# Kernel tuning notes

Hardware: AMD Instinct MI355X
Metric: run time of the kernel (lower is better)

The kernel has to match this reference:

```python
import jax, jax.numpy as jnp
import numpy as np
import math

B = 16          # graphs per batch
N = 2048        # nodes per graph
F_IN = 64       # input node features
E_PER = 32768   # edges per graph
E = B * E_PER
H = 128         # hidden width (fixed by module)
C = 10          # output classes
K = math.ceil(0.8 * N)  # TopKPooling keep count per graph = 1639


def setup_inputs() -> dict:
    key = jax.random.key(0)
    ks = jax.random.split(key, 24)
    x = jax.random.normal(ks[0], (B * N, F_IN), jnp.float32)
    # intra-graph random edges (source->target), global node ids
    gid = jnp.repeat(jnp.arange(B, dtype=jnp.int32), E_PER)
    src = gid * N + jax.random.randint(ks[1], (E,), 0, N, dtype=jnp.int32)
    dst = gid * N + jax.random.randint(ks[2], (E,), 0, N, dtype=jnp.int32)

    def lin_w(k, o, i):
        return jax.random.normal(k, (o, i), jnp.float32) / jnp.sqrt(i)

    inp = dict(x=x, src=src, dst=dst)
    # GraphConv: lin_rel (with bias) on aggregated neighbors + lin_root (no bias)
    inp.update(W1_rel=lin_w(ks[3], H, F_IN), b1=jnp.zeros((H,), jnp.float32), W1_root=lin_w(ks[4], H, F_IN))
    inp.update(W2_rel=lin_w(ks[5], H, H), b2=jnp.zeros((H,), jnp.float32), W2_root=lin_w(ks[6], H, H))
    inp.update(W3_rel=lin_w(ks[7], H, H), b3=jnp.zeros((H,), jnp.float32), W3_root=lin_w(ks[8], H, H))
    inp.update(pool_w=jax.random.normal(ks[9], (H,), jnp.float32) / jnp.sqrt(H))
    inp.update(Wl1=lin_w(ks[10], 128, 256), bl1=jnp.zeros((128,), jnp.float32))
    inp.update(Wl2=lin_w(ks[11], 64, 128), bl2=jnp.zeros((64,), jnp.float32))
    inp.update(Wl3=lin_w(ks[12], C, 64), bl3=jnp.zeros((C,), jnp.float32))
    return inp


def _graph_conv(x, src, dst, W_rel, b, W_root, n_nodes, emask=None):
    # out_i = W_rel @ (sum_{j->i} x_j) + b + W_root @ x_i
    msg = x[src]
    if emask is not None:
        msg = msg * emask[:, None]
    agg = jax.ops.segment_sum(msg, dst, num_segments=n_nodes)
    return agg @ W_rel.T + b + x @ W_root.T


def _global_pools(x, n_per_graph):
    xb = x.reshape(B, n_per_graph, -1)
    return jnp.concatenate([xb.max(axis=1), xb.mean(axis=1)], axis=1)  # [B, 2F]


def reference(x, src, dst, W1_rel, b1, W1_root, W2_rel, b2, W2_root,
              W3_rel, b3, W3_root, pool_w, Wl1, bl1, Wl2, bl2, Wl3, bl3):
    n0 = B * N
    h = jax.nn.relu(_graph_conv(x, src, dst, W1_rel, b1, W1_root, n0))
    x1 = _global_pools(h, N)

    h = jax.nn.relu(_graph_conv(h, src, dst, W2_rel, b2, W2_root, n0))

    # TopKPooling(ratio=0.8): score = tanh(x@w/||w||); keep top-k per graph;
    # kept features scaled by score; edges with a dropped endpoint removed.
    score = jnp.tanh((h @ pool_w) / jnp.linalg.norm(pool_w))  # [B*N]
    top_s, top_i = jax.lax.top_k(score.reshape(B, N), K)      # [B,K]
    perm = (top_i + jnp.arange(B)[:, None] * N).reshape(-1)   # global old ids [B*K]
    h = h[perm] * top_s.reshape(-1)[:, None]                  # [B*K, H]

    n1 = B * K
    new_id = jnp.full((n0,), -1, jnp.int32).at[perm].set(jnp.arange(n1, dtype=jnp.int32))
    ns, nd = new_id[src], new_id[dst]
    keep = ((ns >= 0) & (nd >= 0)).astype(h.dtype)
    ns = jnp.where(ns >= 0, ns, 0)
    nd = jnp.where(nd >= 0, nd, 0)

    x2 = _global_pools(h, K)
    h = jax.nn.relu(_graph_conv(h, ns, nd, W3_rel, b3, W3_root, n1, emask=keep))
    x3 = _global_pools(h, K)

    z = x1 + x2 + x3
    z = jax.nn.relu(z @ Wl1.T + bl1)
    z = jax.nn.relu(z @ Wl2.T + bl2)
    return jax.nn.log_softmax(z @ Wl3.T + bl3, axis=-1)  # [B, C]
```

## Files before the change

kernel.cpp:

```cpp
#include <hip/hip_runtime.h>
#include <hip/hip_bf16.h>
#include <math.h>

#define NB 32768
#define NN 2048
#define BG 16
#define KK 1639
#define KKP 1664
#define N1 (BG*KK)
#define N1P (BG*KKP)
#define EE 524288
#define HH 128
#define FIN 64

using half8 = __attribute__((ext_vector_type(8))) _Float16;
using f32x4 = __attribute__((ext_vector_type(4))) float;

__global__ void deg_kernel(const int* __restrict__ dst, int* deg, int n) {
  int e = blockIdx.x * blockDim.x + threadIdx.x;
  if (e < n) atomicAdd(&deg[dst[e]], 1);
}

__global__ void deg2_kernel(const int* __restrict__ src, const int* __restrict__ dst,
                            const int* __restrict__ new_id, int* deg, int n) {
  int e = blockIdx.x * blockDim.x + threadIdx.x;
  if (e < n) {
    int a = new_id[src[e]], d = new_id[dst[e]];
    if (a >= 0 && d >= 0) atomicAdd(&deg[d], 1);
  }
}

__global__ void exscan_kernel(const int* __restrict__ deg, int* rs, int* cursor, int n) {
  __shared__ int wsum[16];
  __shared__ int carry;
  int t = threadIdx.x;
  int lane = t & 63, wid = t >> 6;
  if (t == 0) carry = 0;
  __syncthreads();
  int ntiles = (n + 4095) >> 12;
  for (int tile = 0; tile < ntiles; ++tile) {
    int idx = (tile << 12) + t * 4;
    int4 v4 = *(const int4*)(deg + idx);
    int v0 = (idx + 0 < n) ? v4.x : 0;
    int v1 = (idx + 1 < n) ? v4.y : 0;
    int v2 = (idx + 2 < n) ? v4.z : 0;
    int v3 = (idx + 3 < n) ? v4.w : 0;
    int s = v0 + v1 + v2 + v3;
    int pre = s;
#pragma unroll
    for (int off = 1; off < 64; off <<= 1) {
      int u = __shfl_up(pre, off, 64);
      if (lane >= off) pre += u;
    }
    if (lane == 63) wsum[wid] = pre;
    __syncthreads();
    int wbase = 0;
#pragma unroll
    for (int ww = 0; ww < 16; ++ww)
      if (ww < wid) wbase += wsum[ww];
    int ex = carry + wbase + (pre - s);
    int4 e4 = make_int4(ex, ex + v0, ex + v0 + v1, ex + v0 + v1 + v2);
    if (idx + 3 < n) {
      *(int4*)(rs + idx) = e4;
      *(int4*)(cursor + idx) = e4;
    } else {
      if (idx + 0 < n) { rs[idx + 0] = e4.x; cursor[idx + 0] = e4.x; }
      if (idx + 1 < n) { rs[idx + 1] = e4.y; cursor[idx + 1] = e4.y; }
      if (idx + 2 < n) { rs[idx + 2] = e4.z; cursor[idx + 2] = e4.z; }
    }
    int tot = 0;
    if (t == 1023) tot = ex + s;
    __syncthreads();
    if (t == 1023) carry = tot;
    __syncthreads();
  }
  if (t == 0) rs[n] = carry;
}

__global__ void scatter_kernel(const int* __restrict__ src, const int* __restrict__ dst,
                               int* cursor, int* csr, int n) {
  int e = blockIdx.x * blockDim.x + threadIdx.x;
  if (e < n) {
    int d = dst[e];
    int p = atomicAdd(&cursor[d], 1);
    csr[p] = src[e];
  }
}

__global__ void scatter2_kernel(const int* __restrict__ src, const int* __restrict__ dst,
                                const int* __restrict__ new_id, int* cursor, int* csr, int n) {
  int e = blockIdx.x * blockDim.x + threadIdx.x;
  if (e < n) {
    int a = new_id[src[e]], d = new_id[dst[e]];
    if (a >= 0 && d >= 0) {
      int p = atomicAdd(&cursor[d], 1);
      csr[p] = a;
    }
  }
}

template <int KD1, int KD2, int POOL, int SCORE>
__global__ __launch_bounds__(512, 4) void conv_mfma(
    const float* __restrict__ feat, const float* __restrict__ xr,
    const int* __restrict__ rs, const int* __restrict__ csr,
    const _Float16* __restrict__ Wh, const _Float16* __restrict__ Wl,
    const float* __restrict__ bias, float* __restrict__ out, int M, int nwg,
    float* __restrict__ pmax, float* __restrict__ psum,
    const float* __restrict__ pw, float* __restrict__ score) {
  constexpr int KTOT = KD1 + KD2;
  constexpr int NSTEP = KTOT / 32;
  constexpr int CPT = KD1 / 32;
  __shared__ _Float16 ah_lds[64 * KTOT];
  __shared__ _Float16 al_lds[64 * KTOT];
  __shared__ float sdot[64][8];
  __shared__ float swsq[8];

  int tid = threadIdx.x;
  int lane = tid & 63, wid = tid >> 6;
  int bq = nwg >> 3, br = nwg & 7, bx = blockIdx.x & 7, bi = blockIdx.x >> 3;
  int swz = (bx < br ? bx * (bq + 1) : br * (bq + 1) + (bx - br) * bq) + bi;
  int row0 = swz * 64;
  int ch0 = wid * 16;
  int col = lane & 15;
  int kseg = (lane >> 4) * 8;

  {
    int gr = tid >> 3;
    int gj = tid & 7;
    int grow = row0 + gr;
    if (grow >= M) grow = M - 1;
    const float4* fbase = (const float4*)feat + gj * CPT;
    int e0 = rs[grow], e1 = rs[grow + 1];
    f32x4 s[CPT];
#pragma unroll
    for (int j = 0; j < CPT; ++j) s[j] = (f32x4){0.f, 0.f, 0.f, 0.f};
    int e = e0;
    for (; e + 3 < e1; e += 4) {
      int c0 = csr[e], c1 = csr[e + 1], c2 = csr[e + 2], c3 = csr[e + 3];
      const float4* p0 = fbase + (size_t)c0 * (KD1 / 4);
      const float4* p1 = fbase + (size_t)c1 * (KD1 / 4);
      const float4* p2 = fbase + (size_t)c2 * (KD1 / 4);
      const float4* p3 = fbase + (size_t)c3 * (KD1 / 4);
      float4 v0[CPT], v1[CPT], v2[CPT], v3[CPT];
#pragma unroll
      for (int j = 0; j < CPT; ++j) { v0[j] = p0[j]; v1[j] = p1[j]; v2[j] = p2[j]; v3[j] = p3[j]; }
#pragma unroll
      for (int j = 0; j < CPT; ++j) {
        s[j] += (f32x4){v0[j].x, v0[j].y, v0[j].z, v0[j].w};
        s[j] += (f32x4){v1[j].x, v1[j].y, v1[j].z, v1[j].w};
        s[j] += (f32x4){v2[j].x, v2[j].y, v2[j].z, v2[j].w};
        s[j] += (f32x4){v3[j].x, v3[j].y, v3[j].z, v3[j].w};
      }
    }
    for (; e < e1; ++e) {
      const float4* p = fbase + (size_t)csr[e] * (KD1 / 4);
#pragma unroll
      for (int j = 0; j < CPT; ++j) {
        float4 v = p[j];
        s[j] += (f32x4){v.x, v.y, v.z, v.w};
      }
    }
    int base = (gr * KTOT + gj * CPT * 4) * 2;
    int sw = (gr & 7) << 4;
#pragma unroll
    for (int h = 0; h < CPT / 2; ++h) {
      half8 vh, vl;
#pragma unroll
      for (int j = 0; j < 8; ++j) {
        float f = s[h * 2 + (j >> 2)][j & 3];
        _Float16 hi = (_Float16)f;
        vh[j] = hi;
        vl[j] = (_Float16)(f - (float)hi);
      }
      int byte = (base + h * 16) ^ sw;
      *(half8*)((char*)ah_lds + byte) = vh;
      *(half8*)((char*)al_lds + byte) = vl;
    }
  }

  for (int idx = tid; idx < 64 * KD2 / 8; idx += 512) {
    int row = idx / (KD2 / 8);
    int kc = (idx % (KD2 / 8)) * 8;
    int grow = row0 + row;
    if (grow >= M) grow = M - 1;
    const float* sp = xr + (size_t)grow * KD2 + kc;
    float4 a0 = *(const float4*)sp;
    float4 a1 = *(const float4*)(sp + 4);
    float av[8] = {a0.x, a0.y, a0.z, a0.w, a1.x, a1.y, a1.z, a1.w};
    half8 vh, vl;
#pragma unroll
    for (int j = 0; j < 8; ++j) {
      _Float16 h = (_Float16)av[j];
      vh[j] = h;
      vl[j] = (_Float16)(av[j] - (float)h);
    }
    int byte = ((row * KTOT + KD1 + kc) * 2) ^ ((row & 7) << 4);
    *(half8*)((char*)ah_lds + byte) = vh;
    *(half8*)((char*)al_lds + byte) = vl;
  }

  size_t wbase = (size_t)(ch0 + col) * KTOT + kseg;
  half8 whc = *(const half8*)(Wh + wbase);
  half8 wlc = *(const half8*)(Wl + wbase);
  __syncthreads();

  f32x4 acc[4];
#pragma unroll
  for (int rf = 0; rf < 4; ++rf) acc[rf] = (f32x4){0.f, 0.f, 0.f, 0.f};
  int r = lane & 15;
#pragma unroll
  for (int s = 0; s < NSTEP; ++s) {
    half8 whn, wln;
    if (s + 1 < NSTEP) {
      whn = *(const half8*)(Wh + wbase + (s + 1) * 32);
      wln = *(const half8*)(Wl + wbase + (s + 1) * 32);
    }
#pragma unroll
    for (int rf = 0; rf < 4; ++rf) {
      int row = rf * 16 + r;
      int byte = ((row * KTOT + s * 32 + kseg) * 2) ^ ((row & 7) << 4);
      half8 a_h = *(const half8*)((const char*)ah_lds + byte);
      half8 a_l = *(const half8*)((const char*)al_lds + byte);
      acc[rf] = __builtin_amdgcn_mfma_f32_16x16x32_f16(a_l, whc, acc[rf], 0, 0, 0);
      acc[rf] = __builtin_amdgcn_mfma_f32_16x16x32_f16(a_h, wlc, acc[rf], 0, 0, 0);
      acc[rf] = __builtin_amdgcn_mfma_f32_16x16x32_f16(a_h, whc, acc[rf], 0, 0, 0);
    }
    if (s + 1 < NSTEP) { whc = whn; wlc = wln; }
  }

  float bv = bias[ch0 + col];
  float cmax = -3.402823466e38f, csum = 0.f;
  float wcol = SCORE ? pw[ch0 + col] : 0.f;
  float pd[4][4];
  int g = 0, rowbase = 0;
  if (POOL == 2) { g = row0 / KKP; rowbase = row0 - g * KKP; }
#pragma unroll
  for (int rf = 0; rf < 4; ++rf) {
    int orow0 = row0 + rf * 16 + (lane >> 4) * 4;
#pragma unroll
    for (int rr = 0; rr < 4; ++rr) {
      int orow = orow0 + rr;
      float v = fmaxf(acc[rf][rr] + bv, 0.f);
      if (orow < M) out[(size_t)orow * HH + ch0 + col] = v;
      if (POOL == 1) { cmax = fmaxf(cmax, v); csum += v; }
      if (POOL == 2) {
        int local = rowbase + rf * 16 + (lane >> 4) * 4 + rr;
        if (local < KK) { cmax = fmaxf(cmax, v); csum += v; }
      }
      if (SCORE) pd[rf][rr] = v * wcol;
    }
  }
  if (POOL) {
    cmax = fmaxf(cmax, __shfl_xor(cmax, 16, 64)); csum += __shfl_xor(csum, 16, 64);
    cmax = fmaxf(cmax, __shfl_xor(cmax, 32, 64)); csum += __shfl_xor(csum, 32, 64);
    if ((lane >> 4) == 0) {
      if (POOL == 1) {
        int gg = row0 >> 11, sb = (row0 & 2047) >> 6;
        pmax[(gg * 32 + sb) * HH + ch0 + col] = cmax;
        psum[(gg * 32 + sb) * HH + ch0 + col] = csum;
      } else {
        int sb = rowbase >> 6;
        pmax[(g * 26 + sb) * HH + ch0 + col] = cmax;
        psum[(g * 26 + sb) * HH + ch0 + col] = csum;
      }
    }
  }
  if (SCORE) {
#pragma unroll
    for (int rf = 0; rf < 4; ++rf)
#pragma unroll
      for (int rr = 0; rr < 4; ++rr) {
        float d = pd[rf][rr];
        d += __shfl_xor(d, 1, 64); d += __shfl_xor(d, 2, 64);
        d += __shfl_xor(d, 4, 64); d += __shfl_xor(d, 8, 64);
        if (col == 0) sdot[rf * 16 + (lane >> 4) * 4 + rr][wid] = d;
      }
    float wsq = wcol * wcol;
    wsq += __shfl_xor(wsq, 1, 64); wsq += __shfl_xor(wsq, 2, 64);
    wsq += __shfl_xor(wsq, 4, 64); wsq += __shfl_xor(wsq, 8, 64);
    if (lane == 0) swsq[wid] = wsq;
    __syncthreads();
    if (tid < 64) {
      float d = 0.f, q = 0.f;
#pragma unroll
      for (int wv = 0; wv < 8; ++wv) { d += sdot[tid][wv]; q += swsq[wv]; }
      score[row0 + tid] = tanhf(d * rsqrtf(q));
    }
  }
}

__global__ void prep_weights_f16(const float* __restrict__ W1_rel, const float* __restrict__ W1_root,
                                 const float* __restrict__ W2_rel, const float* __restrict__ W2_root,
                                 const float* __restrict__ W3_rel, const float* __restrict__ W3_root,
                                 _Float16* wh1, _Float16* wl1, _Float16* wh2, _Float16* wl2,
                                 _Float16* wh3, _Float16* wl3) {
  int idx = blockIdx.x * blockDim.x + threadIdx.x;
  float v;
  _Float16* ph;
  _Float16* pl;
  int j;
  if (idx < 128 * 128) {
    j = idx;
    int o = j >> 7, k = j & 127;
    v = (k < 64) ? W1_rel[o * 64 + k] : W1_root[o * 64 + (k - 64)];
    ph = wh1; pl = wl1;
  } else if (idx < 128 * 128 + 128 * 256) {
    j = idx - 128 * 128;
    int o = j >> 8, k = j & 255;
    v = (k < 128) ? W2_rel[o * 128 + k] : W2_root[o * 128 + (k - 128)];
    ph = wh2; pl = wl2;
  } else if (idx < 128 * 128 + 2 * 128 * 256) {
    j = idx - 128 * 128 - 128 * 256;
    int o = j >> 8, k = j & 255;
    v = (k < 128) ? W3_rel[o * 128 + k] : W3_root[o * 128 + (k - 128)];
    ph = wh3; pl = wl3;
  } else {
    return;
  }
  _Float16 h = (_Float16)v;
  ph[j] = h;
  pl[j] = (_Float16)(v - (float)h);
}

__global__ void topk_kernel(const float* __restrict__ score, int* perm) {
  __shared__ unsigned long long k[NN];
  int b = blockIdx.x;
  int tid = threadIdx.x;
  for (int i = tid; i < NN; i += 1024) {
    float s = score[b * NN + i];
    unsigned u = __float_as_uint(s);
    u = (u & 0x80000000u) ? ~u : (u | 0x80000000u);
    unsigned long long key = ((unsigned long long)u << 32) | (unsigned)(NN - 1 - i);
    k[i] = ~key;
  }
  __syncthreads();
  for (int kk = 2; kk <= NN; kk <<= 1) {
    for (int j = kk >> 1; j > 0; j >>= 1) {
      for (int t = tid; t < NN; t += 1024) {
        int ixj = t ^ j;
        if (ixj > t) {
          bool up = ((t & kk) == 0);
          unsigned long long a = k[t], c = k[ixj];
          if ((a > c) == up) { k[t] = c; k[ixj] = a; }
        }
      }
      __syncthreads();
    }
  }
  for (int j = tid; j < KK; j += 1024) {
    unsigned long long key = ~k[j];
    int i = (NN - 1) - (int)(key & 0xffffffffu);
    perm[b * KK + j] = b * NN + i;
  }
}

__global__ void h3_kernel(const float4* __restrict__ h2, const int* __restrict__ perm,
                          const float* __restrict__ score, float4* __restrict__ h3,
                          int* __restrict__ new_id) {
  int idx = blockIdx.x * blockDim.x + threadIdx.x;
  if (idx < N1 * 32) {
    int g = idx >> 5, c = idx & 31;
    int b = g / KK, j = g - b * KK;
    int p = perm[g];
    if (c == 0) new_id[p] = b * KKP + j;
    float s = score[p];
    float4 v = h2[(size_t)p * 32 + c];
    v.x *= s; v.y *= s; v.z *= s; v.w *= s;
    h3[(size_t)(b * KKP + j) * 32 + c] = v;
  }
}

__global__ void pool2_kernel(const float* __restrict__ h, float* pmax, float* psum) {
  int b = blockIdx.x / 26, s = blockIdx.x % 26;
  int f = threadIdx.x;
  int r0 = s * 64, r1 = min(KK, r0 + 64);
  float m = -3.402823466e38f, sum = 0.f;
  for (int r = r0; r < r1; ++r) {
    float v = h[(size_t)(b * KKP + r) * HH + f];
    m = fmaxf(m, v);
    sum += v;
  }
  pmax[(b * 26 + s) * HH + f] = m;
  psum[(b * 26 + s) * HH + f] = sum;
}

__global__ void mlp_kernel(const float* __restrict__ pm1, const float* __restrict__ ps1,
                           const float* __restrict__ pm2, const float* __restrict__ ps2,
                           const float* __restrict__ pm3, const float* __restrict__ ps3,
                           const float* __restrict__ Wl1, const float* __restrict__ bl1,
                           const float* __restrict__ Wl2, const float* __restrict__ bl2,
                           const float* __restrict__ Wl3, const float* __restrict__ bl3,
                           float* out) {
  __shared__ float z[256], a1[128], a2[64], a3[10], red[2];
  int b = blockIdx.x, t = threadIdx.x;
  float m1 = -3.402823466e38f, m2 = m1, m3 = m1;
  float s1 = 0.f, s2 = 0.f, s3 = 0.f;
  for (int s = 0; s < 32; ++s) {
    int o = (b * 32 + s) * 128 + t;
    m1 = fmaxf(m1, pm1[o]); s1 += ps1[o];
  }
  for (int s = 0; s < 26; ++s) {
    int o = (b * 26 + s) * 128 + t;
    m2 = fmaxf(m2, pm2[o]); s2 += ps2[o];
    m3 = fmaxf(m3, pm3[o]); s3 += ps3[o];
  }
  z[t] = m1 + m2 + m3;
  z[128 + t] = s1 * (1.f / NN) + (s2 + s3) * (1.f / KK);
  __syncthreads();
  {
    float acc = bl1[t];
    for (int q = 0; q < 256; ++q) acc = fmaf(Wl1[t * 256 + q], z[q], acc);
    a1[t] = fmaxf(acc, 0.f);
  }
  __syncthreads();
  if (t < 64) {
    float acc = bl2[t];
    for (int q = 0; q < 128; ++q) acc = fmaf(Wl2[t * 128 + q], a1[q], acc);
    a2[t] = fmaxf(acc, 0.f);
  }
  __syncthreads();
  if (t < 10) {
    float acc = bl3[t];
    for (int q = 0; q < 64; ++q) acc = fmaf(Wl3[t * 64 + q], a2[q], acc);
    a3[t] = acc;
  }
  __syncthreads();
  if (t == 0) {
    float m = a3[0];
    for (int i = 1; i < 10; ++i) m = fmaxf(m, a3[i]);
    float s = 0.f;
    for (int i = 0; i < 10; ++i) s += expf(a3[i] - m);
    red[0] = m;
    red[1] = logf(s);
  }
  __syncthreads();
  if (t < 10) out[b * 10 + t] = a3[t] - red[0] - red[1];
}

extern "C" void kernel_launch(void* const* d_in, const int* in_sizes, int n_in,
                              void* d_out, int out_size, void* d_ws, size_t ws_size,
                              hipStream_t stream) {
  const float* x       = (const float*)d_in[0];
  const int*   src     = (const int*)d_in[1];
  const int*   dst     = (const int*)d_in[2];
  const float* W1_rel  = (const float*)d_in[3];
  const float* b1      = (const float*)d_in[4];
  const float* W1_root = (const float*)d_in[5];
  const float* W2_rel  = (const float*)d_in[6];
  const float* b2      = (const float*)d_in[7];
  const float* W2_root = (const float*)d_in[8];
  const float* W3_rel  = (const float*)d_in[9];
  const float* b3      = (const float*)d_in[10];
  const float* W3_root = (const float*)d_in[11];
  const float* pool_w  = (const float*)d_in[12];
  const float* Wl1     = (const float*)d_in[13];
  const float* bl1     = (const float*)d_in[14];
  const float* Wl2     = (const float*)d_in[15];
  const float* bl2     = (const float*)d_in[16];
  const float* Wl3     = (const float*)d_in[17];
  const float* bl3     = (const float*)d_in[18];
  float* out = (float*)d_out;

  char* w = (char*)d_ws;
  size_t off = 0;
  auto alloc = [&](size_t bytes) -> char* {
    off = (off + 255) & ~(size_t)255;
    char* p = w + off;
    off += bytes;
    return p;
  };
  int* degs     = (int*)alloc((NB + N1P + 4096) * 4);
  int* deg1     = degs;
  int* deg2     = degs + NB;
  int* rs1      = (int*)alloc((NB + 1) * 4);
  int* cursor1  = (int*)alloc(NB * 4);
  int* csr1     = (int*)alloc((size_t)EE * 4);
  int* rs2      = (int*)alloc((N1P + 1) * 4);
  int* cursor2  = (int*)alloc(N1P * 4);
  int* csr2     = (int*)alloc((size_t)EE * 4);
  int* new_id   = (int*)alloc(NB * 4);
  int* perm     = (int*)alloc(N1 * 4);
  _Float16* wh1 = (_Float16*)alloc(128 * 128 * 2);
  _Float16* wl1 = (_Float16*)alloc(128 * 128 * 2);
  _Float16* wh2 = (_Float16*)alloc(128 * 256 * 2);
  _Float16* wl2 = (_Float16*)alloc(128 * 256 * 2);
  _Float16* wh3 = (_Float16*)alloc(128 * 256 * 2);
  _Float16* wl3 = (_Float16*)alloc(128 * 256 * 2);
  float* bufA   = (float*)alloc((size_t)NB * HH * 4);
  float* bufB   = (float*)alloc((size_t)NB * HH * 4);
  float* score  = (float*)alloc(NB * 4);
  float* pm1    = (float*)alloc(BG * 32 * HH * 4);
  float* ps1    = (float*)alloc(BG * 32 * HH * 4);
  float* pm2    = (float*)alloc(BG * 26 * HH * 4);
  float* ps2    = (float*)alloc(BG * 26 * HH * 4);
  float* pm3    = (float*)alloc(BG * 26 * HH * 4);
  float* ps3    = (float*)alloc(BG * 26 * HH * 4);
  if (off > ws_size) return;

  const int TB = 256;
  const int egrid = (EE + TB - 1) / TB;

  hipMemsetAsync(degs, 0, (NB + N1P + 4096) * 4, stream);
  hipMemsetAsync(new_id, 0xFF, NB * 4, stream);

  prep_weights_f16<<<(128 * 128 + 2 * 128 * 256 + TB - 1) / TB, TB, 0, stream>>>(
      W1_rel, W1_root, W2_rel, W2_root, W3_rel, W3_root, wh1, wl1, wh2, wl2, wh3, wl3);

  deg_kernel<<<egrid, TB, 0, stream>>>(dst, deg1, EE);
  exscan_kernel<<<1, 1024, 0, stream>>>(deg1, rs1, cursor1, NB);
  scatter_kernel<<<egrid, TB, 0, stream>>>(src, dst, cursor1, csr1, EE);

  conv_mfma<64, 64, 1, 0><<<NB / 64, 512, 0, stream>>>(
      x, x, rs1, csr1, wh1, wl1, b1, bufA, NB, NB / 64, pm1, ps1, nullptr, nullptr);

  conv_mfma<128, 128, 0, 1><<<NB / 64, 512, 0, stream>>>(
      bufA, bufA, rs1, csr1, wh2, wl2, b2, bufB, NB, NB / 64, nullptr, nullptr, pool_w, score);

  topk_kernel<<<BG, 1024, 0, stream>>>(score, perm);
  h3_kernel<<<(N1 * 32 + TB - 1) / TB, TB, 0, stream>>>((const float4*)bufB, perm, score,
                                                        (float4*)bufA, new_id);
  pool2_kernel<<<BG * 26, 128, 0, stream>>>(bufA, pm2, ps2);

  deg2_kernel<<<egrid, TB, 0, stream>>>(src, dst, new_id, deg2, EE);
  exscan_kernel<<<1, 1024, 0, stream>>>(deg2, rs2, cursor2, N1P);
  scatter2_kernel<<<egrid, TB, 0, stream>>>(src, dst, new_id, cursor2, csr2, EE);

  conv_mfma<128, 128, 2, 0><<<N1P / 64, 512, 0, stream>>>(
      bufA, bufA, rs2, csr2, wh3, wl3, b3, bufB, N1P, N1P / 64, pm3, ps3, nullptr, nullptr);

  mlp_kernel<<<BG, 128, 0, stream>>>(pm1, ps1, pm2, ps2, pm3, ps3,
                                     Wl1, bl1, Wl2, bl2, Wl3, bl3, out);
}
```

Before: 275.0 us.

## Restructure neighbor gather so each wave cooperatively aggregates rows with coalesced loads

Replaces the per-thread gather, where 8 threads per row each summed a fixed slice of features serially over all edges, with a wave-per-8-rows scheme. In the new scheme lanes split into feature chunks and edge subgroups, and partial sums are combined with cross-lane shuffles. Each edge's feature row is now read by contiguous lanes, which coalesces loads and spreads the edge loop across lanes to cut per-row latency on long adjacency lists. The cost is more shuffles and wave-serialized row processing, and some lanes sit idle when a row has few edges.

Result: no change. 277.1 us (+0.7%).

```diff
diff --git a/kernel.cpp b/kernel.cpp
--- a/kernel.cpp
+++ b/kernel.cpp
@@ -14,6 +14,7 @@
 #define FIN 64
 
 using half8 = __attribute__((ext_vector_type(8))) _Float16;
+using half4 = __attribute__((ext_vector_type(4))) _Float16;
 using f32x4 = __attribute__((ext_vector_type(4))) float;
 
 __global__ void deg_kernel(const int* __restrict__ dst, int* deg, int n) {
@@ -109,7 +110,6 @@
     const float* __restrict__ pw, float* __restrict__ score) {
   constexpr int KTOT = KD1 + KD2;
   constexpr int NSTEP = KTOT / 32;
-  constexpr int CPT = KD1 / 32;
   __shared__ _Float16 ah_lds[64 * KTOT];
   __shared__ _Float16 al_lds[64 * KTOT];
   __shared__ float sdot[64][8];
@@ -125,56 +125,53 @@
   int kseg = (lane >> 4) * 8;
 
   {
-    int gr = tid >> 3;
-    int gj = tid & 7;
-    int grow = row0 + gr;
-    if (grow >= M) grow = M - 1;
-    const float4* fbase = (const float4*)feat + gj * CPT;
-    int e0 = rs[grow], e1 = rs[grow + 1];
-    f32x4 s[CPT];
-#pragma unroll
-    for (int j = 0; j < CPT; ++j) s[j] = (f32x4){0.f, 0.f, 0.f, 0.f};
-    int e = e0;
-    for (; e + 3 < e1; e += 4) {
-      int c0 = csr[e], c1 = csr[e + 1], c2 = csr[e + 2], c3 = csr[e + 3];
-      const float4* p0 = fbase + (size_t)c0 * (KD1 / 4);
-      const float4* p1 = fbase + (size_t)c1 * (KD1 / 4);
-      const float4* p2 = fbase + (size_t)c2 * (KD1 / 4);
-      const float4* p3 = fbase + (size_t)c3 * (KD1 / 4);
-      float4 v0[CPT], v1[CPT], v2[CPT], v3[CPT];
-#pragma unroll
-      for (int j = 0; j < CPT; ++j) { v0[j] = p0[j]; v1[j] = p1[j]; v2[j] = p2[j]; v3[j] = p3[j]; }
-#pragma unroll
-      for (int j = 0; j < CPT; ++j) {
-        s[j] += (f32x4){v0[j].x, v0[j].y, v0[j].z, v0[j].w};
-        s[j] += (f32x4){v1[j].x, v1[j].y, v1[j].z, v1[j].w};
-        s[j] += (f32x4){v2[j].x, v2[j].y, v2[j].z, v2[j].w};
-        s[j] += (f32x4){v3[j].x, v3[j].y, v3[j].z, v3[j].w};
-      }
-    }
-    for (; e < e1; ++e) {
-      const float4* p = fbase + (size_t)csr[e] * (KD1 / 4);
-#pragma unroll
-      for (int j = 0; j < CPT; ++j) {
-        float4 v = p[j];
-        s[j] += (f32x4){v.x, v.y, v.z, v.w};
-      }
-    }
-    int base = (gr * KTOT + gj * CPT * 4) * 2;
-    int sw = (gr & 7) << 4;
-#pragma unroll
-    for (int h = 0; h < CPT / 2; ++h) {
-      half8 vh, vl;
-#pragma unroll
-      for (int j = 0; j < 8; ++j) {
-        float f = s[h * 2 + (j >> 2)][j & 3];
-        _Float16 hi = (_Float16)f;
-        vh[j] = hi;
-        vl[j] = (_Float16)(f - (float)hi);
-      }
-      int byte = (base + h * 16) ^ sw;
-      *(half8*)((char*)ah_lds + byte) = vh;
-      *(half8*)((char*)al_lds + byte) = vl;
+    constexpr int CH = KD1 / 4;
+    constexpr int EPW = 64 / CH;
+    int sub = lane / CH;
+    int ch = lane % CH;
+    const float4* feat4 = (const float4*)feat;
+#pragma unroll
+    for (int rr = 0; rr < 8; ++rr) {
+      int gr = wid * 8 + rr;
+      int grow = row0 + gr;
+      if (grow >= M) grow = M - 1;
+      int e0 = rs[grow], e1 = rs[grow + 1];
+      f32x4 a0 = {0.f, 0.f, 0.f, 0.f}, a1 = a0, a2 = a0, a3 = a0;
+      int e = e0 + sub;
+      for (; e + 3 * EPW < e1; e += 4 * EPW) {
+        int c0 = csr[e], c1 = csr[e + EPW], c2 = csr[e + 2 * EPW], c3 = csr[e + 3 * EPW];
+        float4 v0 = feat4[(size_t)c0 * CH + ch];
+        float4 v1 = feat4[(size_t)c1 * CH + ch];
+        float4 v2 = feat4[(size_t)c2 * CH + ch];
+        float4 v3 = feat4[(size_t)c3 * CH + ch];
+        a0 += (f32x4){v0.x, v0.y, v0.z, v0.w};
+        a1 += (f32x4){v1.x, v1.y, v1.z, v1.w};
+        a2 += (f32x4){v2.x, v2.y, v2.z, v2.w};
+        a3 += (f32x4){v3.x, v3.y, v3.z, v3.w};
+      }
+      for (; e < e1; e += EPW) {
+        float4 v = feat4[(size_t)csr[e] * CH + ch];
+        a0 += (f32x4){v.x, v.y, v.z, v.w};
+      }
+      f32x4 s = (a0 + a1) + (a2 + a3);
+      if (EPW == 4) {
+#pragma unroll
+        for (int j = 0; j < 4; ++j) s[j] += __shfl_xor(s[j], 16, 64);
+      }
+#pragma unroll
+      for (int j = 0; j < 4; ++j) s[j] += __shfl_xor(s[j], 32, 64);
+      if (sub == 0) {
+        half4 hi, lo;
+#pragma unroll
+        for (int j = 0; j < 4; ++j) {
+          _Float16 h = (_Float16)s[j];
+          hi[j] = h;
+          lo[j] = (_Float16)(s[j] - (float)h);
+        }
+        int byte = ((gr * KTOT + ch * 4) * 2) ^ ((gr & 7) << 4);
+        *(half4*)((char*)ah_lds + byte) = hi;
+        *(half4*)((char*)al_lds + byte) = lo;
+      }
     }
   }
 
```
